# Kernel tuning notes

Measured on AMD Instinct MI355X. Metric: run time of the kernel, lower is better.

## Reference

```python
import jax, jax.numpy as jnp
import numpy as np

DIM = 128; DSTATE = 8; DCONV = 4; DTRANK = 8
B = 2; T = 48; H = 16; W = 16
EPS = 1e-5

def _ln(x, w, b):
    mu = jnp.mean(x, -1, keepdims=True)
    var = jnp.mean(jnp.square(x - mu), -1, keepdims=True)
    return (x - mu) * jax.lax.rsqrt(var + EPS) * w + b

def _causal_dwconv(x, w, b):
    # x: [B,L,D], w: [D,K] depthwise, causal padding K-1 on the left
    xt = jnp.transpose(x, (0, 2, 1))  # [B,D,L]
    out = jax.lax.conv_general_dilated(
        xt, w[:, None, :], (1,), [(w.shape[-1] - 1, 0)],
        dimension_numbers=('NCH', 'OIH', 'NCH'),
        feature_group_count=x.shape[-1])
    return jnp.transpose(out + b[:, None], (0, 2, 1))

def _selective_scan(u, dt, A, Bc, Cc, Dp):
    # u, dt: [B,L,D]; A: [D,N]; Bc, Cc: [B,L,N]; Dp: [D]
    dA = jnp.exp(dt[..., None] * A)                          # [B,L,D,N]
    dBx = dt[..., None] * Bc[:, :, None, :] * u[..., None]   # [B,L,D,N]
    def combine(c1, c2):
        a1, b1 = c1; a2, b2 = c2
        return a1 * a2, a2 * b1 + b2
    _, hs = jax.lax.associative_scan(combine, (dA, dBx), axis=1)
    return jnp.einsum('bldn,bln->bld', hs, Cc) + u * Dp

def _bimamba(xn, in_w, conv_w, conv_b, xp_w, dt_w, dt_b, A_log, Dp, out_w):
    # xn: [B,L,DIM]; direction-stacked params have leading axis 2 (fwd/bwd)
    xz = xn @ in_w.T                      # [B,L,2*DIM]
    xh, z = jnp.split(xz, 2, axis=-1)
    acc = 0.0
    for d in range(2):
        xi = xh if d == 0 else xh[:, ::-1]
        zi = z if d == 0 else z[:, ::-1]
        xc = jax.nn.silu(_causal_dwconv(xi, conv_w[d], conv_b[d]))
        proj = xc @ xp_w[d].T             # [B,L,DTRANK+2*DSTATE]
        dtr, Bc, Cc = jnp.split(proj, [DTRANK, DTRANK + DSTATE], axis=-1)
        dt = jax.nn.softplus(dtr @ dt_w[d].T + dt_b[d])
        A = -jnp.exp(A_log[d])
        y = _selective_scan(xc, dt, A, Bc, Cc, Dp[d]) * jax.nn.silu(zi)
        acc = acc + (y if d == 0 else y[:, ::-1])
    return acc @ out_w.T

def setup_inputs():
    key = jax.random.key(0)
    ks = jax.random.split(key, 10)
    s = 0.1
    return {
        "x": jax.random.normal(ks[0], (B, DIM, T, H, W), jnp.float32),
        "norm1_w": jnp.ones((DIM,), jnp.float32),
        "norm1_b": jnp.zeros((DIM,), jnp.float32),
        "norm2_w": jnp.ones((DIM,), jnp.float32),
        "norm2_b": jnp.zeros((DIM,), jnp.float32),
        "subln_w": jnp.ones((DIM,), jnp.float32),
        "subln_b": jnp.zeros((DIM,), jnp.float32),
        "lambda_q": jax.random.normal(ks[1], (DIM,), jnp.float32) * s,
        "in_proj_w": jax.random.normal(ks[2], (2, 2 * DIM, DIM), jnp.float32) * s,
        "conv_w": jax.random.normal(ks[3], (2, 2, DIM, DCONV), jnp.float32) * s,
        "conv_b": jax.random.normal(ks[4], (2, 2, DIM), jnp.float32) * s,
        "x_proj_w": jax.random.normal(ks[5], (2, 2, DTRANK + 2 * DSTATE, DIM), jnp.float32) * s,
        "dt_proj_w": jax.random.normal(ks[6], (2, 2, DIM, DTRANK), jnp.float32) * s,
        "dt_proj_b": jax.random.normal(ks[7], (2, 2, DIM), jnp.float32) * s,
        "A_log": jnp.broadcast_to(jnp.log(jnp.arange(1, DSTATE + 1, dtype=jnp.float32)), (2, 2, DIM, DSTATE)) + 0.0,
        "D": jnp.ones((2, 2, DIM), jnp.float32),
        "out_proj_w": jax.random.normal(ks[8], (2, DIM, DIM), jnp.float32) * s,
    }

def reference(x, norm1_w, norm1_b, norm2_w, norm2_b, subln_w, subln_b,
              lambda_q, in_proj_w, conv_w, conv_b, x_proj_w,
              dt_proj_w, dt_proj_b, A_log, D, out_proj_w):
    Bsz, C = x.shape[0], x.shape[1]
    Tt, Hh, Ww = x.shape[2], x.shape[3], x.shape[4]
    L = Tt * Hh * Ww
    x_flat = jnp.transpose(x.reshape(Bsz, C, L), (0, 2, 1))  # [B,L,C]
    x_norm = _ln(x_flat, norm1_w, norm1_b)
    y1 = _bimamba(x_norm, in_proj_w[0], conv_w[0], conv_b[0], x_proj_w[0],
                  dt_proj_w[0], dt_proj_b[0], A_log[0], D[0], out_proj_w[0])
    y2 = _bimamba(x_norm, in_proj_w[1], conv_w[1], conv_b[1], x_proj_w[1],
                  dt_proj_w[1], dt_proj_b[1], A_log[1], D[1], out_proj_w[1])
    lam = jax.nn.sigmoid(jnp.sum(lambda_q))
    attn = _ln(y1 - lam * y2, subln_w, subln_b)
    out = _ln(x_flat + attn, norm2_w, norm2_b)
    return jnp.transpose(out, (0, 2, 1)).reshape(Bsz, C, Tt, Hh, Ww)
```

## Files before the change

kernel.cpp:

```cpp
#include <hip/hip_runtime.h>
#include <math.h>

#define DIMC 128
#define LSEQ 12288
#define NB 2
#define BLR 24576
#define EPSV 1e-5f
#define NCH 256
#define LC 48
#define KP 132

typedef __bf16 bf16x8 __attribute__((ext_vector_type(8)));
typedef __attribute__((ext_vector_type(4))) float f4_t;

__device__ __forceinline__ float sigf(float x){ return 1.f/(1.f+__expf(-x)); }
__device__ __forceinline__ float softplusf(float x){
    return fmaxf(x,0.f) + __logf(1.f + __expf(-fabsf(x)));
}
__device__ __forceinline__ float bf2f(unsigned short u){
    union { unsigned int i; float f; } v; v.i = ((unsigned int)u) << 16; return v.f;
}
__device__ __forceinline__ unsigned short f2bf(float f){
    union { float f; unsigned int i; } v; v.f = f;
    unsigned int b = v.i + 0x7FFFu + ((v.i >> 16) & 1u);
    return (unsigned short)(b >> 16);
}
__device__ __forceinline__ bf16x8 ld_frag8(const unsigned short* p){
    union { uint2 u[2]; bf16x8 v; } r;
    r.u[0] = *(const uint2*)(p);
    r.u[1] = *(const uint2*)(p+4);
    return r.v;
}
__device__ __forceinline__ bf16x8 ld_frag16g(const unsigned short* p){
    union { uint4 u; bf16x8 v; } r; r.u = *(const uint4*)p; return r.v;
}

__global__ void k_lam(const float* __restrict__ lq, float* __restrict__ lam){
    int lane = threadIdx.x;
    float v = lq[lane] + lq[lane+64];
    for (int m = 32; m; m >>= 1) v += __shfl_xor(v, m);
    if (lane == 0) *lam = 1.f/(1.f+__expf(-v));
}

__global__ void k_wall(const float* __restrict__ dtw, const float* __restrict__ xpw,
                       unsigned short* __restrict__ wallb){
    int inst = blockIdx.x, j = blockIdx.y, k = threadIdx.x;
    const float* xp = xpw + (size_t)inst*24*128;
    float v;
    if (j < 128){
        const float* dw = dtw + (size_t)inst*128*8 + (size_t)j*8;
        v = 0.f;
        #pragma unroll
        for (int r = 0; r < 8; r++) v += dw[r]*xp[r*128 + k];
    } else {
        v = xp[(8 + (j-128))*128 + k];
    }
    wallb[((size_t)inst*144 + j)*128 + k] = f2bf(v);
}

__global__ __launch_bounds__(256) void k_prep(const float* __restrict__ wi, const float* __restrict__ ow,
    unsigned short* __restrict__ wib, unsigned short* __restrict__ owb){
    int idx = (blockIdx.x*256 + threadIdx.x)*4;
    const float* src; unsigned short* dst; int off;
    if (idx < 65536){ src = wi;  dst = wib; off = idx; }
    else            { src = ow;  dst = owb; off = idx - 65536; }
    float4 v = *(const float4*)&src[off];
    ushort4 o; o.x=f2bf(v.x); o.y=f2bf(v.y); o.z=f2bf(v.z); o.w=f2bf(v.w);
    *(ushort4*)&dst[off] = o;
}

__global__ __launch_bounds__(256) void k_normT(const float* __restrict__ x,
    const float* __restrict__ w1, const float* __restrict__ b1, unsigned short* __restrict__ xn)
{
    __shared__ float t[64*129];
    __shared__ float red1[256], red2[256];
    __shared__ float stt[128];
    const int bb = blockIdx.x / 192;
    const int l0 = (blockIdx.x % 192) * 64;
    const int tid = threadIdx.x;
    const int li = tid & 63, cg = tid >> 6;
    #pragma unroll
    for (int p = 0; p < 32; p++){
        int c = p*4 + cg;
        t[li*129 + c] = x[(size_t)bb*DIMC*LSEQ + (size_t)c*LSEQ + l0 + li];
    }
    __syncthreads();
    {
        int r = tid >> 2, qg = tid & 3;
        float s = 0.f, s2 = 0.f;
        #pragma unroll
        for (int j = 0; j < 32; j++){ float v = t[r*129 + qg*32 + j]; s += v; s2 += v*v; }
        red1[qg*64 + r] = s; red2[qg*64 + r] = s2;
    }
    __syncthreads();
    if (tid < 64){
        float s = 0.f, s2 = 0.f;
        #pragma unroll
        for (int g = 0; g < 4; g++){ s += red1[g*64 + tid]; s2 += red2[g*64 + tid]; }
        float mu = s*(1.f/128.f);
        float var = s2*(1.f/128.f) - mu*mu;
        stt[tid*2] = mu; stt[tid*2+1] = rsqrtf(var + EPSV);
    }
    __syncthreads();
    const int c2 = (tid & 63)*2, lg = tid >> 6;
    #pragma unroll
    for (int p = 0; p < 16; p++){
        int l = p*4 + lg;
        float mu = stt[l*2], rs = stt[l*2+1];
        float v0 = (t[l*129 + c2    ] - mu)*rs*w1[c2    ] + b1[c2    ];
        float v1 = (t[l*129 + c2 + 1] - mu)*rs*w1[c2 + 1] + b1[c2 + 1];
        unsigned int o = (unsigned int)f2bf(v0) | ((unsigned int)f2bf(v1) << 16);
        *(unsigned int*)&xn[(size_t)(bb*LSEQ + l0 + l)*DIMC + c2] = o;
    }
}

__global__ __launch_bounds__(256,4) void k_inproj(const unsigned short* __restrict__ xn,
    const unsigned short* __restrict__ wib, unsigned short* __restrict__ xz)
{
    __shared__ __align__(16) unsigned short As[128*KP];
    const int row0 = blockIdx.x * 128;
    const int j0   = blockIdx.y * 128;
    const int tid = threadIdx.x;
    #pragma unroll
    for (int p = 0; p < 8; p++){
        int idx = p*256 + tid; int li = idx >> 4; int g = (idx & 15)*8;
        uint4 va = *(const uint4*)&xn[(size_t)(row0+li)*DIMC + g];
        *(uint2*)&As[li*KP + g]     = make_uint2(va.x, va.y);
        *(uint2*)&As[li*KP + g + 4] = make_uint2(va.z, va.w);
    }
    __syncthreads();
    const int lane = tid & 63, w = tid >> 6;
    const int m15 = lane & 15, q = lane >> 4;
    f4_t zf = {0.f,0.f,0.f,0.f};
    f4_t acc[2][8];
    #pragma unroll
    for (int i = 0; i < 2; i++)
        #pragma unroll
        for (int j = 0; j < 8; j++) acc[i][j] = zf;
    #pragma unroll
    for (int ks = 0; ks < 4; ks++){
        int k0 = ks*32 + q*8;
        bf16x8 a0 = ld_frag8(&As[(w*32      + m15)*KP + k0]);
        bf16x8 a1 = ld_frag8(&As[(w*32 + 16 + m15)*KP + k0]);
        #pragma unroll
        for (int nt = 0; nt < 8; nt++){
            bf16x8 b = ld_frag16g(&wib[(size_t)(j0 + nt*16 + m15)*DIMC + k0]);
            acc[0][nt] = __builtin_amdgcn_mfma_f32_16x16x32_bf16(a0, b, acc[0][nt], 0,0,0);
            acc[1][nt] = __builtin_amdgcn_mfma_f32_16x16x32_bf16(a1, b, acc[1][nt], 0,0,0);
        }
    }
    __syncthreads();
    unsigned short* ep = As;
    #pragma unroll
    for (int mi = 0; mi < 2; mi++)
        #pragma unroll
        for (int nt = 0; nt < 8; nt++){
            int row = w*32 + mi*16 + q*4;
            int col = nt*16 + m15;
            #pragma unroll
            for (int i = 0; i < 4; i++)
                ep[(row+i)*KP + col] = f2bf(acc[mi][nt][i]);
        }
    __syncthreads();
    #pragma unroll
    for (int p = 0; p < 8; p++){
        int idx = p*256 + tid; int li = idx >> 4; int g = (idx & 15)*8;
        uint2 u0 = *(const uint2*)&ep[li*KP + g];
        uint2 u1 = *(const uint2*)&ep[li*KP + g + 4];
        uint4 o; o.x=u0.x; o.y=u0.y; o.z=u1.x; o.w=u1.y;
        *(uint4*)&xz[(size_t)(row0+li)*512 + j0 + g] = o;
    }
}

__global__ __launch_bounds__(256) void k_conv(const unsigned short* __restrict__ xz,
    const float* __restrict__ cw, const float* __restrict__ cb, unsigned short* __restrict__ xc)
{
    __shared__ unsigned short tile[70][144];
    const int bid = blockIdx.x;
    const int lt = bid % 192;
    const int bb = (bid/192) % NB;
    const int m  = bid / (192*NB);
    const int l0 = lt * 64;
    const int tid = threadIdx.x;
    for (int idx = tid; idx < 70*16; idx += 256){
        int r = idx >> 4, cq = idx & 15;
        int l = l0 - 3 + r;
        uint4 v = make_uint4(0,0,0,0);
        if (l >= 0 && l < LSEQ)
            v = *(const uint4*)&xz[((size_t)(bb*LSEQ + l))*512 + m*256 + cq*8];
        *(uint4*)&tile[r][cq*8] = v;
    }
    __syncthreads();
    const int dimi = tid & 127, lg = tid >> 7;
    float w0a[4], w1a[4];
    #pragma unroll
    for (int k = 0; k < 4; k++){
        w0a[k] = cw[((size_t)(m*2+0)*DIMC + dimi)*4 + k];
        w1a[k] = cw[((size_t)(m*2+1)*DIMC + dimi)*4 + k];
    }
    const float b0 = cb[(m*2+0)*DIMC + dimi];
    const float b1v = cb[(m*2+1)*DIMC + dimi];
    for (int p = 0; p < 32; p++){
        int li = p*2 + lg;
        float t0 = bf2f(tile[li  ][dimi]);
        float t1 = bf2f(tile[li+1][dimi]);
        float t2 = bf2f(tile[li+2][dimi]);
        float t3 = bf2f(tile[li+3][dimi]);
        float t4 = bf2f(tile[li+4][dimi]);
        float t5 = bf2f(tile[li+5][dimi]);
        float t6 = bf2f(tile[li+6][dimi]);
        float v0 = b0  + w0a[0]*t0 + w0a[1]*t1 + w0a[2]*t2 + w0a[3]*t3;
        float v1 = b1v + w1a[3]*t3 + w1a[2]*t4 + w1a[1]*t5 + w1a[0]*t6;
        v0 = v0 * sigf(v0);
        v1 = v1 * sigf(v1);
        xc[(((size_t)(m*2+0)*NB + bb)*LSEQ + l0 + li)*DIMC + dimi] = f2bf(v0);
        xc[(((size_t)(m*2+1)*NB + bb)*LSEQ + l0 + li)*DIMC + dimi] = f2bf(v1);
    }
}

__global__ __launch_bounds__(256,4) void k_xproj(const unsigned short* __restrict__ xc,
    const unsigned short* __restrict__ wallb, const float* __restrict__ dtb,
    unsigned short* __restrict__ dty, float* __restrict__ bcb)
{
    __shared__ __align__(16) unsigned short As[128*KP];
    const int row0 = blockIdx.x * 128;
    const int ib   = blockIdx.y;
    const int inst = ib >> 1;
    const int tid = threadIdx.x;
    const size_t abase = (size_t)ib * LSEQ * DIMC;
    #pragma unroll
    for (int p = 0; p < 8; p++){
        int idx = p*256 + tid; int li = idx >> 4; int g = (idx & 15)*8;
        uint4 va = *(const uint4*)&xc[abase + (size_t)(row0+li)*DIMC + g];
        *(uint2*)&As[li*KP + g]     = make_uint2(va.x, va.y);
        *(uint2*)&As[li*KP + g + 4] = make_uint2(va.z, va.w);
    }
    __syncthreads();
    const int lane = tid & 63, w = tid >> 6;
    const int m15 = lane & 15, q = lane >> 4;
    f4_t zf = {0.f,0.f,0.f,0.f};
    f4_t acc[2][9];
    #pragma unroll
    for (int i = 0; i < 2; i++)
        #pragma unroll
        for (int j = 0; j < 9; j++) acc[i][j] = zf;
    #pragma unroll
    for (int ks = 0; ks < 4; ks++){
        int k0 = ks*32 + q*8;
        bf16x8 a0 = ld_frag8(&As[(w*32      + m15)*KP + k0]);
        bf16x8 a1 = ld_frag8(&As[(w*32 + 16 + m15)*KP + k0]);
        #pragma unroll
        for (int nt = 0; nt < 9; nt++){
            bf16x8 b = ld_frag16g(&wallb[((size_t)inst*144 + nt*16 + m15)*DIMC + k0]);
            acc[0][nt] = __builtin_amdgcn_mfma_f32_16x16x32_bf16(a0, b, acc[0][nt], 0,0,0);
            acc[1][nt] = __builtin_amdgcn_mfma_f32_16x16x32_bf16(a1, b, acc[1][nt], 0,0,0);
        }
    }
    #pragma unroll
    for (int mi = 0; mi < 2; mi++){
        int row = w*32 + mi*16 + q*4;
        #pragma unroll
        for (int i = 0; i < 4; i++)
            bcb[((size_t)ib*LSEQ + row0 + row + i)*16 + m15] = acc[mi][8][i];
    }
    __syncthreads();
    unsigned short* ep = As;
    #pragma unroll
    for (int nt = 0; nt < 8; nt++){
        int col = nt*16 + m15;
        float bias = dtb[inst*DIMC + col];
        #pragma unroll
        for (int mi = 0; mi < 2; mi++){
            int row = w*32 + mi*16 + q*4;
            #pragma unroll
            for (int i = 0; i < 4; i++)
                ep[(row+i)*KP + col] = f2bf(softplusf(acc[mi][nt][i] + bias));
        }
    }
    __syncthreads();
    #pragma unroll
    for (int p = 0; p < 8; p++){
        int idx = p*256 + tid; int li = idx >> 4; int g = (idx & 15)*8;
        uint2 u0 = *(const uint2*)&ep[li*KP + g];
        uint2 u1 = *(const uint2*)&ep[li*KP + g + 4];
        uint4 o; o.x=u0.x; o.y=u0.y; o.z=u1.x; o.w=u1.y;
        *(uint4*)&dty[abase + (size_t)(row0+li)*DIMC + g] = o;
    }
}

__global__ __launch_bounds__(128) void k_scan1(const unsigned short* __restrict__ dt,
    const unsigned short* __restrict__ xc, const float* __restrict__ bcb,
    const float* __restrict__ alog, float* __restrict__ st)
{
    const int ib = blockIdx.x & 7;
    const int c  = blockIdx.x >> 3;
    const int inst = ib >> 1;
    const int d = inst & 1;
    const int tid = threadIdx.x;
    float Av[8];
    #pragma unroll
    for (int n = 0; n < 8; n++) Av[n] = -__expf(alog[((size_t)inst*DIMC + tid)*8 + n]);
    const size_t rbase = (size_t)ib*LSEQ*DIMC;
    float Ac[8], Bc[8];
    #pragma unroll
    for (int n = 0; n < 8; n++){ Ac[n] = 1.f; Bc[n] = 0.f; }
    #pragma unroll 4
    for (int s = 0; s < LC; s++){
        int j = c*LC + s;
        int l = d ? (LSEQ-1-j) : j;
        size_t ro = rbase + (size_t)l*DIMC + tid;
        float dtv = bf2f(dt[ro]);
        float uv  = bf2f(xc[ro]);
        const float* bp = bcb + ((size_t)ib*LSEQ + l)*16;
        float4 bA = *(const float4*)bp;
        float4 bB = *(const float4*)(bp+4);
        float bv[8] = {bA.x,bA.y,bA.z,bA.w,bB.x,bB.y,bB.z,bB.w};
        float du = dtv*uv;
        #pragma unroll
        for (int n = 0; n < 8; n++){
            float a = __expf(dtv*Av[n]);
            Bc[n] = a*Bc[n] + du*bv[n];
            Ac[n] *= a;
        }
    }
    float* so = st + (((size_t)ib*NCH + c)*DIMC + tid)*16;
    #pragma unroll
    for (int n = 0; n < 8; n++){ so[n] = Ac[n]; so[8+n] = Bc[n]; }
}

__global__ __launch_bounds__(256) void k_scan2(const float* __restrict__ st, float* __restrict__ hst){
    int gid = blockIdx.x*256 + threadIdx.x;
    int ib = gid >> 10;
    int r  = gid & 1023;
    int dim = r >> 3, n = r & 7;
    float Bp = 0.f;
    for (int c = 0; c < NCH; c++){
        size_t o = (((size_t)ib*NCH + c)*DIMC + dim)*16;
        float A = st[o+n], Bv = st[o+8+n];
        hst[(((size_t)ib*NCH + c)*DIMC + dim)*8 + n] = Bp;
        Bp = A*Bp + Bv;
    }
}

__global__ __launch_bounds__(128) void k_scan3(unsigned short* __restrict__ dty,
    const unsigned short* __restrict__ xc, const float* __restrict__ bcb,
    const unsigned short* __restrict__ xz, const float* __restrict__ hst,
    const float* __restrict__ alog, const float* __restrict__ dvec)
{
    const int ib = blockIdx.x & 7;
    const int c  = blockIdx.x >> 3;
    const int inst = ib >> 1, bb = ib & 1;
    const int m = inst >> 1, d = inst & 1;
    const int tid = threadIdx.x;
    float Av[8];
    #pragma unroll
    for (int n = 0; n < 8; n++) Av[n] = -__expf(alog[((size_t)inst*DIMC + tid)*8 + n]);
    const float Dv = dvec[inst*DIMC + tid];
    float h[8];
    #pragma unroll
    for (int n = 0; n < 8; n++) h[n] = hst[(((size_t)ib*NCH + c)*DIMC + tid)*8 + n];
    const size_t rbase = (size_t)ib*LSEQ*DIMC;
    const size_t zbase = (size_t)bb*LSEQ*512 + m*256 + 128;
    #pragma unroll 2
    for (int s = 0; s < LC; s++){
        int j = c*LC + s;
        int l = d ? (LSEQ-1-j) : j;
        size_t ro = rbase + (size_t)l*DIMC + tid;
        float dtv = bf2f(dty[ro]);
        float uv  = bf2f(xc[ro]);
        const float* bp = bcb + ((size_t)ib*LSEQ + l)*16;
        float4 bA = *(const float4*)bp;
        float4 bB = *(const float4*)(bp+4);
        float4 cA = *(const float4*)(bp+8);
        float4 cB = *(const float4*)(bp+12);
        float bv[8] = {bA.x,bA.y,bA.z,bA.w,bB.x,bB.y,bB.z,bB.w};
        float cv[8] = {cA.x,cA.y,cA.z,cA.w,cB.x,cB.y,cB.z,cB.w};
        float du = dtv*uv;
        float y = uv*Dv;
        #pragma unroll
        for (int n = 0; n < 8; n++){
            float a = __expf(dtv*Av[n]);
            h[n] = a*h[n] + du*bv[n];
            y += h[n]*cv[n];
        }
        float zv = bf2f(xz[zbase + (size_t)l*512 + tid]);
        y *= zv * sigf(zv);
        dty[ro] = f2bf(y);
    }
}

__global__ __launch_bounds__(256,3) void k_final(const unsigned short* __restrict__ y,
    const unsigned short* __restrict__ owb, const float* __restrict__ x, const float* __restrict__ lamp,
    const float* __restrict__ sw, const float* __restrict__ sb,
    const float* __restrict__ n2w, const float* __restrict__ n2b, float* __restrict__ outp)
{
    __shared__ __align__(16) char smem[52480];
    unsigned short* Ast = (unsigned short*)smem;
    float* yt            = (float*)smem;
    unsigned short* xtb  = (unsigned short*)(smem + 33024);
    float* red1          = (float*)(smem + 49920);
    float* red2          = (float*)(smem + 50944);
    float* stt           = (float*)(smem + 51968);
    const int bb = blockIdx.y;
    const int l0 = blockIdx.x * 64;
    const int tid = threadIdx.x;
    const float lam = *lamp;
    #pragma unroll
    for (int p = 0; p < 8; p++){
        int idx = p*256 + tid; int mm = idx >> 10; int li = (idx >> 4) & 63; int g = (idx & 15)*8;
        uint4 vf = *(const uint4*)&y[(((size_t)(mm*2+0)*NB + bb)*LSEQ + l0 + li)*DIMC + g];
        uint4 vb = *(const uint4*)&y[(((size_t)(mm*2+1)*NB + bb)*LSEQ + l0 + li)*DIMC + g];
        const unsigned short* uf = (const unsigned short*)&vf;
        const unsigned short* ub = (const unsigned short*)&vb;
        unsigned short o[8];
        #pragma unroll
        for (int j = 0; j < 8; j++) o[j] = f2bf(bf2f(uf[j]) + bf2f(ub[j]));
        *(uint2*)&Ast[(mm*64 + li)*KP + g]     = *(uint2*)&o[0];
        *(uint2*)&Ast[(mm*64 + li)*KP + g + 4] = *(uint2*)&o[4];
    }
    __syncthreads();
    const int lane = tid & 63, w = tid >> 6;
    const int m15 = lane & 15, q = lane >> 4;
    f4_t zf = {0.f,0.f,0.f,0.f};
    f4_t acc[2][8];
    #pragma unroll
    for (int i = 0; i < 2; i++)
        #pragma unroll
        for (int j = 0; j < 8; j++) acc[i][j] = zf;
    #pragma unroll
    for (int ks = 0; ks < 4; ks++){
        int k0 = ks*32 + q*8;
        bf16x8 a0 = ld_frag8(&Ast[(       w*16 + m15)*KP + k0]);
        bf16x8 a1 = ld_frag8(&Ast[(64   + w*16 + m15)*KP + k0]);
        #pragma unroll
        for (int nt = 0; nt < 8; nt++){
            bf16x8 b0 = ld_frag16g(&owb[((size_t)0*DIMC + nt*16 + m15)*DIMC + k0]);
            bf16x8 b1 = ld_frag16g(&owb[((size_t)1*DIMC + nt*16 + m15)*DIMC + k0]);
            acc[0][nt] = __builtin_amdgcn_mfma_f32_16x16x32_bf16(a0, b0, acc[0][nt], 0,0,0);
            acc[1][nt] = __builtin_amdgcn_mfma_f32_16x16x32_bf16(a1, b1, acc[1][nt], 0,0,0);
        }
    }
    __syncthreads();
    #pragma unroll
    for (int nt = 0; nt < 8; nt++){
        int row = w*16 + q*4;
        int col = nt*16 + m15;
        #pragma unroll
        for (int i = 0; i < 4; i++)
            yt[(row+i)*129 + col] = acc[0][nt][i] - lam*acc[1][nt][i];
    }
    {
        const int li = tid & 63, cg = tid >> 6;
        #pragma unroll
        for (int p = 0; p < 32; p++){
            int c = p*4 + cg;
            xtb[li*132 + c] = f2bf(x[(size_t)bb*DIMC*LSEQ + (size_t)c*LSEQ + l0 + li]);
        }
    }
    __syncthreads();
    const int r = tid & 63, g = tid >> 6;
    float s = 0.f, s2 = 0.f;
    #pragma unroll
    for (int k = 0; k < 32; k++){ float v = yt[r*129 + g*32 + k]; s += v; s2 += v*v; }
    red1[g*64 + r] = s; red2[g*64 + r] = s2;
    __syncthreads();
    if (tid < 64){
        float ss = 0.f, ss2 = 0.f;
        #pragma unroll
        for (int gg = 0; gg < 4; gg++){ ss += red1[gg*64 + tid]; ss2 += red2[gg*64 + tid]; }
        float mu = ss*(1.f/128.f);
        float var = ss2*(1.f/128.f) - mu*mu;
        stt[tid*2] = mu; stt[tid*2+1] = rsqrtf(var + EPSV);
    }
    __syncthreads();
    float mu1 = stt[r*2], rs1 = stt[r*2+1];
    s = 0.f; s2 = 0.f;
    #pragma unroll
    for (int k = 0; k < 32; k++){
        int c = g*32 + k;
        float v = (yt[r*129+c] - mu1)*rs1*sw[c] + sb[c] + bf2f(xtb[r*132+c]);
        yt[r*129+c] = v;
        s += v; s2 += v*v;
    }
    __syncthreads();
    red1[g*64 + r] = s; red2[g*64 + r] = s2;
    __syncthreads();
    if (tid < 64){
        float ss = 0.f, ss2 = 0.f;
        #pragma unroll
        for (int gg = 0; gg < 4; gg++){ ss += red1[gg*64 + tid]; ss2 += red2[gg*64 + tid]; }
        float mu = ss*(1.f/128.f);
        float var = ss2*(1.f/128.f) - mu*mu;
        stt[tid*2] = mu; stt[tid*2+1] = rsqrtf(var + EPSV);
    }
    __syncthreads();
    float mu2 = stt[r*2], rs2 = stt[r*2+1];
    #pragma unroll
    for (int k = 0; k < 32; k++){
        int c = g*32 + k;
        float o = (yt[r*129+c] - mu2)*rs2*n2w[c] + n2b[c];
        outp[(size_t)bb*DIMC*LSEQ + (size_t)c*LSEQ + l0 + r] = o;
    }
}

extern "C" void kernel_launch(void* const* d_in, const int* in_sizes, int n_in,
                              void* d_out, int out_size, void* d_ws, size_t ws_size,
                              hipStream_t stream)
{
    const float* x    = (const float*)d_in[0];
    const float* n1w  = (const float*)d_in[1];
    const float* n1b  = (const float*)d_in[2];
    const float* n2w  = (const float*)d_in[3];
    const float* n2b  = (const float*)d_in[4];
    const float* slw  = (const float*)d_in[5];
    const float* slb  = (const float*)d_in[6];
    const float* lq   = (const float*)d_in[7];
    const float* wi   = (const float*)d_in[8];
    const float* cw   = (const float*)d_in[9];
    const float* cb   = (const float*)d_in[10];
    const float* xpw  = (const float*)d_in[11];
    const float* dtw  = (const float*)d_in[12];
    const float* dtb  = (const float*)d_in[13];
    const float* alog = (const float*)d_in[14];
    const float* dvec = (const float*)d_in[15];
    const float* ow   = (const float*)d_in[16];

    float* ws = (float*)d_ws;
    unsigned short* xn    = (unsigned short*)(ws);
    unsigned short* xz    = (unsigned short*)(ws + 1572864);
    unsigned short* xc    = (unsigned short*)(ws + 7864320);
    unsigned short* dty   = (unsigned short*)(ws + 14155776);
    float*          bcb   = ws + 20447232;
    float*          st1   = ws + 22020096;
    float*          hst   = ws + 26214400;
    unsigned short* wallb = (unsigned short*)(ws + 28311552);
    unsigned short* wib   = (unsigned short*)(ws + 28348416);
    unsigned short* owb   = (unsigned short*)(ws + 28381184);
    float*          lam   = ws + 28397568;

    k_lam   <<<1, 64, 0, stream>>>(lq, lam);
    k_wall  <<<dim3(4,144), 128, 0, stream>>>(dtw, xpw, wallb);
    k_prep  <<<96, 256, 0, stream>>>(wi, ow, wib, owb);
    k_normT <<<384, 256, 0, stream>>>(x, n1w, n1b, xn);
    k_inproj<<<dim3(192, 4), 256, 0, stream>>>(xn, wib, xz);
    k_conv  <<<2*NB*(LSEQ/64), 256, 0, stream>>>(xz, cw, cb, xc);
    k_xproj <<<dim3(96, 8), 256, 0, stream>>>(xc, wallb, dtb, dty, bcb);
    k_scan1 <<<8*NCH, 128, 0, stream>>>(dty, xc, bcb, alog, st1);
    k_scan2 <<<32, 256, 0, stream>>>(st1, hst);
    k_scan3 <<<8*NCH, 128, 0, stream>>>(dty, xc, bcb, xz, hst, alog, dvec);
    k_final <<<dim3(192, 2), 256, 0, stream>>>(dty, owb, x, lam, slw, slb, n2w, n2b, (float*)d_out);
}
```

Measured before the change: 283.1 us.

## Shorten scan chunks, fold lambda into weight prep, reuse scan state buffer

The chunked selective scan now uses 384 chunks of 32 steps instead of 256 of 48, giving more blocks for the scan kernels. The scalar lambda kernel is merged into the weight-prep kernel to remove one launch. The chunk prefix states are written in place into the scan buffer rather than a separate one, and exp is replaced by exp2 with A pre-scaled by log2(e). The chunk-combine kernel's serial loop gets longer, and scan3's unroll factor is raised.

```diff
diff --git a/kernel.cpp b/kernel.cpp
--- a/kernel.cpp
+++ b/kernel.cpp
@@ -6,8 +6,8 @@
 #define NB 2
 #define BLR 24576
 #define EPSV 1e-5f
-#define NCH 256
-#define LC 48
+#define NCH 384
+#define LC 32
 #define KP 132
 
 typedef __bf16 bf16x8 __attribute__((ext_vector_type(8)));
@@ -35,15 +35,9 @@
     union { uint4 u; bf16x8 v; } r; r.u = *(const uint4*)p; return r.v;
 }
 
-__global__ void k_lam(const float* __restrict__ lq, float* __restrict__ lam){
-    int lane = threadIdx.x;
-    float v = lq[lane] + lq[lane+64];
-    for (int m = 32; m; m >>= 1) v += __shfl_xor(v, m);
-    if (lane == 0) *lam = 1.f/(1.f+__expf(-v));
-}
-
 __global__ void k_wall(const float* __restrict__ dtw, const float* __restrict__ xpw,
-                       unsigned short* __restrict__ wallb){
+                       const float* __restrict__ lq,
+                       unsigned short* __restrict__ wallb, float* __restrict__ lam){
     int inst = blockIdx.x, j = blockIdx.y, k = threadIdx.x;
     const float* xp = xpw + (size_t)inst*24*128;
     float v;
@@ -56,6 +50,11 @@
         v = xp[(8 + (j-128))*128 + k];
     }
     wallb[((size_t)inst*144 + j)*128 + k] = f2bf(v);
+    if (inst == 0 && j == 0 && k < 64){
+        float s = lq[k] + lq[k+64];
+        for (int m = 32; m; m >>= 1) s += __shfl_xor(s, m);
+        if (k == 0) *lam = 1.f/(1.f+__expf(-s));
+    }
 }
 
 __global__ __launch_bounds__(256) void k_prep(const float* __restrict__ wi, const float* __restrict__ ow,
@@ -299,7 +298,8 @@
     const int tid = threadIdx.x;
     float Av[8];
     #pragma unroll
-    for (int n = 0; n < 8; n++) Av[n] = -__expf(alog[((size_t)inst*DIMC + tid)*8 + n]);
+    for (int n = 0; n < 8; n++)
+        Av[n] = -__expf(alog[((size_t)inst*DIMC + tid)*8 + n]) * 1.44269504089f;
     const size_t rbase = (size_t)ib*LSEQ*DIMC;
     float Ac[8], Bc[8];
     #pragma unroll
@@ -318,7 +318,7 @@
         float du = dtv*uv;
         #pragma unroll
         for (int n = 0; n < 8; n++){
-            float a = __expf(dtv*Av[n]);
+            float a = exp2f(dtv*Av[n]);
             Bc[n] = a*Bc[n] + du*bv[n];
             Ac[n] *= a;
         }
@@ -328,7 +328,7 @@
     for (int n = 0; n < 8; n++){ so[n] = Ac[n]; so[8+n] = Bc[n]; }
 }
 
-__global__ __launch_bounds__(256) void k_scan2(const float* __restrict__ st, float* __restrict__ hst){
+__global__ __launch_bounds__(256) void k_scan2(float* __restrict__ st){
     int gid = blockIdx.x*256 + threadIdx.x;
     int ib = gid >> 10;
     int r  = gid & 1023;
@@ -337,14 +337,14 @@
     for (int c = 0; c < NCH; c++){
         size_t o = (((size_t)ib*NCH + c)*DIMC + dim)*16;
         float A = st[o+n], Bv = st[o+8+n];
-        hst[(((size_t)ib*NCH + c)*DIMC + dim)*8 + n] = Bp;
+        st[o+n] = Bp;
         Bp = A*Bp + Bv;
     }
 }
 
 __global__ __launch_bounds__(128) void k_scan3(unsigned short* __restrict__ dty,
     const unsigned short* __restrict__ xc, const float* __restrict__ bcb,
-    const unsigned short* __restrict__ xz, const float* __restrict__ hst,
+    const unsigned short* __restrict__ xz, const float* __restrict__ st,
     const float* __restrict__ alog, const float* __restrict__ dvec)
 {
     const int ib = blockIdx.x & 7;
@@ -354,14 +354,16 @@
     const int tid = threadIdx.x;
     float Av[8];
     #pragma unroll
-    for (int n = 0; n < 8; n++) Av[n] = -__expf(alog[((size_t)inst*DIMC + tid)*8 + n]);
+    for (int n = 0; n < 8; n++)
+        Av[n] = -__expf(alog[((size_t)inst*DIMC + tid)*8 + n]) * 1.44269504089f;
     const float Dv = dvec[inst*DIMC + tid];
     float h[8];
-    #pragma unroll
-    for (int n = 0; n < 8; n++) h[n] = hst[(((size_t)ib*NCH + c)*DIMC + tid)*8 + n];
+    const float* hp = st + (((size_t)ib*NCH + c)*DIMC + tid)*16;
+    #pragma unroll
+    for (int n = 0; n < 8; n++) h[n] = hp[n];
     const size_t rbase = (size_t)ib*LSEQ*DIMC;
     const size_t zbase = (size_t)bb*LSEQ*512 + m*256 + 128;
-    #pragma unroll 2
+    #pragma unroll 4
     for (int s = 0; s < LC; s++){
         int j = c*LC + s;
         int l = d ? (LSEQ-1-j) : j;
@@ -379,7 +381,7 @@
         float y = uv*Dv;
         #pragma unroll
         for (int n = 0; n < 8; n++){
-            float a = __expf(dtv*Av[n]);
+            float a = exp2f(dtv*Av[n]);
             h[n] = a*h[n] + du*bv[n];
             y += h[n]*cv[n];
         }
@@ -532,21 +534,19 @@
     unsigned short* dty   = (unsigned short*)(ws + 14155776);
     float*          bcb   = ws + 20447232;
     float*          st1   = ws + 22020096;
-    float*          hst   = ws + 26214400;
     unsigned short* wallb = (unsigned short*)(ws + 28311552);
     unsigned short* wib   = (unsigned short*)(ws + 28348416);
     unsigned short* owb   = (unsigned short*)(ws + 28381184);
     float*          lam   = ws + 28397568;
 
-    k_lam   <<<1, 64, 0, stream>>>(lq, lam);
-    k_wall  <<<dim3(4,144), 128, 0, stream>>>(dtw, xpw, wallb);
+    k_wall  <<<dim3(4,144), 128, 0, stream>>>(dtw, xpw, lq, wallb, lam);
     k_prep  <<<96, 256, 0, stream>>>(wi, ow, wib, owb);
     k_normT <<<384, 256, 0, stream>>>(x, n1w, n1b, xn);
     k_inproj<<<dim3(192, 4), 256, 0, stream>>>(xn, wib, xz);
     k_conv  <<<2*NB*(LSEQ/64), 256, 0, stream>>>(xz, cw, cb, xc);
     k_xproj <<<dim3(96, 8), 256, 0, stream>>>(xc, wallb, dtb, dty, bcb);
     k_scan1 <<<8*NCH, 128, 0, stream>>>(dty, xc, bcb, alog, st1);
-    k_scan2 <<<32, 256, 0, stream>>>(st1, hst);
-    k_scan3 <<<8*NCH, 128, 0, stream>>>(dty, xc, bcb, xz, hst, alog, dvec);
+    k_scan2 <<<32, 256, 0, stream>>>(st1);
+    k_scan3 <<<8*NCH, 128, 0, stream>>>(dty, xc, bcb, xz, st1, alog, dvec);
     k_final <<<dim3(192, 2), 256, 0, stream>>>(dty, owb, x, lam, slw, slb, n2w, n2b, (float*)d_out);
 }
```

Result: slower. 297.4 us (+5.0%).
